# Kernel optimization log

Measured on AMD Instinct MI355X. Metric: run time of the kernel, lower is better.

Reference implementation:

```python
import jax, jax.numpy as jnp
import numpy as np

B, CIN, COUT, K, E, H, W = 32, 128, 256, 3, 8, 64, 64


def setup_inputs() -> dict:
    key = jax.random.key(0)
    k1, k2, k3, k4 = jax.random.split(key, 4)
    x = jax.random.normal(k1, (B, CIN, H, W), dtype=jnp.float32)
    expert_weight = jax.random.normal(k2, (E, COUT, CIN, K, K), dtype=jnp.float32)
    # nn.Linear(in_channels, num_experts): weight [E, CIN], bias [E]
    bound = 1.0 / np.sqrt(CIN)
    routing_w = jax.random.uniform(k3, (E, CIN), minval=-bound, maxval=bound, dtype=jnp.float32)
    routing_b = jax.random.uniform(k4, (E,), minval=-bound, maxval=bound, dtype=jnp.float32)
    return {"x": x, "expert_weight": expert_weight, "routing_w": routing_w, "routing_b": routing_b}


def reference(x, expert_weight, routing_w, routing_b):
    # routing: global-avg-pool -> linear -> softmax over experts
    pooled = x.mean(axis=(2, 3))                             # [B, CIN]
    logits = pooled @ routing_w.T + routing_b                # [B, E]
    rweights = jax.nn.softmax(logits, axis=-1)               # [B, E]
    # per-sample combined conv weights: [B, COUT, CIN, K, K]
    cw = jnp.einsum('be,eoikl->boikl', rweights, expert_weight)

    def conv_one(xi, wi):
        # xi: [CIN, H, W], wi: [COUT, CIN, K, K]; VALID conv, stride 1
        return jax.lax.conv_general_dilated(
            xi[None], wi, window_strides=(1, 1), padding='VALID',
            dimension_numbers=('NCHW', 'OIHW', 'NCHW'))[0]

    return jax.vmap(conv_one)(x, cw)                         # [B, COUT, H-K+1, W-K+1]
```

## Files before the change

### kernel.cpp

```cpp
#include <hip/hip_runtime.h>
#include <hip/hip_bf16.h>


#define CC_B    32
#define CC_CIN  128
#define CC_COUT 256
#define CC_NP   3844
#define CC_NT   18

typedef __attribute__((ext_vector_type(8))) short bf16x8;
typedef __attribute__((ext_vector_type(16))) float f32x16;

__global__ void cc_nhwc(const float* __restrict__ x, __hip_bfloat16* __restrict__ xn,
                        float* __restrict__ psum) {
    const int b = blockIdx.x >> 6, y = blockIdx.x & 63;
    __shared__ float lds[64 * 129];
    __shared__ float sred[256];
    const int t = threadIdx.x;
    const float* src = x + (size_t)b * CC_CIN * 4096 + y * 64;
#pragma unroll
    for (int i = 0; i < 32; ++i) {
        const int idx = i * 256 + t;
        const int cin = idx >> 6, xx = idx & 63;
        lds[xx * 129 + cin] = src[(size_t)cin * 4096 + xx];
    }
    __syncthreads();
    __hip_bfloat16* dst = xn + ((size_t)b * 4096 + y * 64) * CC_CIN;
#pragma unroll
    for (int j = 0; j < 4; ++j) {
        const int cidx = j * 256 + t;
        const int xx = cidx >> 4, c8 = (cidx & 15) * 8;
        union { __hip_bfloat16 h[8]; uint4 v; } u;
#pragma unroll
        for (int jj = 0; jj < 8; ++jj) u.h[jj] = __float2bfloat16(lds[xx * 129 + c8 + jj]);
        *reinterpret_cast<uint4*>(dst + (size_t)xx * CC_CIN + c8) = u.v;
    }
    const int cin = t & 127, xh = (t >> 7) * 32;
    float s = 0.f;
#pragma unroll
    for (int xx = 0; xx < 32; ++xx) s += lds[(xh + xx) * 129 + cin];
    sred[t] = s;
    __syncthreads();
    if (t < 128) psum[((size_t)b * 64 + y) * CC_CIN + t] = sred[t] + sred[t + 128];
}

__global__ void cc_route(const float* __restrict__ psum,
                         const float* __restrict__ rw_w,
                         const float* __restrict__ rw_b,
                         float* __restrict__ rweights) {
    const int b = blockIdx.x, c = threadIdx.x;
    __shared__ float pl[128];
    __shared__ float lg[8];
    const float* p = psum + (size_t)b * 64 * CC_CIN + c;
    float s = 0.f;
#pragma unroll 8
    for (int y = 0; y < 64; ++y) s += p[(size_t)y * CC_CIN];
    pl[c] = s * (1.f / 4096.f);
    __syncthreads();
    if (c < 8) {
        const float* w = rw_w + c * CC_CIN;
        float a = rw_b[c];
#pragma unroll 8
        for (int i = 0; i < CC_CIN; ++i) a += pl[i] * w[i];
        lg[c] = a;
    }
    __syncthreads();
    if (c == 0) {
        float m = lg[0];
#pragma unroll
        for (int e = 1; e < 8; ++e) m = fmaxf(m, lg[e]);
        float ex[8], sm = 0.f;
#pragma unroll
        for (int e = 0; e < 8; ++e) { ex[e] = __expf(lg[e] - m); sm += ex[e]; }
#pragma unroll
        for (int e = 0; e < 8; ++e) rweights[b * 8 + e] = ex[e] / sm;
    }
}

__global__ void cc_combine(const float* __restrict__ ew,
                           const float* __restrict__ rw,
                           __hip_bfloat16* __restrict__ cw) {
    const int t9 = blockIdx.x >> 8;
    const int cout = blockIdx.x & 255;
    const int cin = threadIdx.x;
    __shared__ float rws[256];
    rws[cin] = rw[cin];
    rws[cin + 128] = rw[cin + 128];
    __syncthreads();
    float wv[8];
    const size_t base = ((size_t)cout * CC_CIN + cin) * 9 + t9;
#pragma unroll
    for (int e = 0; e < 8; ++e) wv[e] = ew[base + (size_t)e * (CC_COUT * CC_CIN * 9)];
#pragma unroll 4
    for (int b = 0; b < CC_B; ++b) {
        float acc = 0.f;
#pragma unroll
        for (int e = 0; e < 8; ++e) acc += rws[b * 8 + e] * wv[e];
        cw[(((size_t)b * 9 + t9) * CC_COUT + cout) * CC_CIN + cin] = __float2bfloat16(acc);
    }
}

__device__ __forceinline__ void gload_lds16(const void* g, void* l) {
    __builtin_amdgcn_global_load_lds(
        (const __attribute__((address_space(1))) unsigned int*)g,
        (__attribute__((address_space(3))) unsigned int*)l, 16, 0, 0);
}

__global__ __launch_bounds__(256) void cc_conv(
    const __hip_bfloat16* __restrict__ xn,
    const __hip_bfloat16* __restrict__ cw,
    float* __restrict__ out)
{
    __shared__ __align__(16) char smem[65536];
    const int l   = blockIdx.x;
    const int xcd = l & 7, li = l >> 3;
    const int b   = 4 * xcd + li / 62;
    const int r2  = li % 62;
    const int nt  = r2 >> 1, mt = r2 & 1;
    const int m0  = mt * 128;
    const int n0  = nt * 124;
    const int y0  = 2 * nt;

    const int tid = threadIdx.x;
    const int wid = tid >> 6, lane = tid & 63;
    const int waveM = wid >> 1, waveN = wid & 1;

    f32x16 acc[2][2];
#pragma unroll
    for (int i = 0; i < 2; ++i)
#pragma unroll
        for (int j = 0; j < 2; ++j)
#pragma unroll
            for (int v = 0; v < 16; ++v) acc[i][j][v] = 0.f;

    const __hip_bfloat16* cwb = cw + (size_t)b * 9 * CC_COUT * CC_CIN;
    const __hip_bfloat16* xnb = xn + (size_t)b * 4096 * CC_CIN;

    const int aRow = (wid >> 1) * 64 + lane;
    int laOff[4];
#pragma unroll
    for (int i = 0; i < 4; ++i)
        laOff[i] = (m0 + aRow) * CC_CIN + (i * 2 + (wid & 1)) * 8;
    auto stageA = [&](int t) {
        const int h = t / 9, t9 = t - 9 * h;
        const int aoff = t9 * (CC_COUT * CC_CIN) + h * 64;
        char* Ab = smem + (t & 1) * 16384 + (wid >> 1) * 1024;
#pragma unroll
        for (int i = 0; i < 4; ++i)
            gload_lds16(cwb + aoff + laOff[i], Ab + (i * 2 + (wid & 1)) * 2048);
    };

    char* Bres = smem + 32768;
    const int lbOff = ((y0 + wid) * 64 + lane) * CC_CIN;
    auto stageB = [&](int h) {
        char* Bb = Bres + wid * 1024;
#pragma unroll
        for (int i = 0; i < 8; ++i)
            gload_lds16(xnb + lbOff + i * 8 + h * 64, Bb + i * 4096);
    };

    const int l31 = lane & 31, q2 = lane >> 5;

    int pixB[2];
#pragma unroll
    for (int nf = 0; nf < 2; ++nf) {
        int c = nf * 32 + l31;
        if (c > 61) c = 61;
        pixB[nf] = waveN * 64 + c;
    }

    stageB(0);
    stageA(0);
    stageA(1);

#pragma unroll
    for (int t = 0; t < CC_NT; ++t) {
        const int h = t / 9, t9 = t - 9 * h;
        const int kyx = (t9 / 3) * 64 + (t9 - 3 * (t9 / 3));
        const char* Ab = smem + (t & 1) * 16384;

        if (t < CC_NT - 1) asm volatile("s_waitcnt vmcnt(4)" ::: "memory");
        else               asm volatile("s_waitcnt vmcnt(0)" ::: "memory");
        asm volatile("s_barrier" ::: "memory");

        bf16x8 af[2][4], bf[2][4];
#pragma unroll
        for (int ks = 0; ks < 4; ++ks) {
            const int c = ks * 2 + q2;
#pragma unroll
            for (int mf = 0; mf < 2; ++mf) {
                const int r = waveM * 64 + mf * 32 + l31;
                af[mf][ks] = *(const bf16x8*)(Ab + c * 2048 + r * 16);
            }
#pragma unroll
            for (int nf = 0; nf < 2; ++nf) {
                const int row = pixB[nf] + kyx;
                bf[nf][ks] = *(const bf16x8*)(Bres + c * 4096 + row * 16);
            }
        }
        __builtin_amdgcn_s_setprio(1);
#pragma unroll
        for (int ks = 0; ks < 4; ++ks)
#pragma unroll
            for (int mf = 0; mf < 2; ++mf)
#pragma unroll
                for (int nf = 0; nf < 2; ++nf)
                    acc[mf][nf] = __builtin_amdgcn_mfma_f32_32x32x16_bf16(
                        af[mf][ks], bf[nf][ks], acc[mf][nf], 0, 0, 0);
        __builtin_amdgcn_s_setprio(0);

        asm volatile("s_waitcnt lgkmcnt(0)" ::: "memory");
        asm volatile("s_barrier" ::: "memory");
        if (t == 8) stageB(1);
        if (t + 2 < CC_NT) stageA(t + 2);
    }

#pragma unroll
    for (int mf = 0; mf < 2; ++mf) {
#pragma unroll
        for (int nf = 0; nf < 2; ++nf) {
            const int c2 = nf * 32 + l31;
            if (c2 < 62) {
                const int p = n0 + waveN * 62 + c2;
#pragma unroll
                for (int g = 0; g < 4; ++g) {
                    const int crow = m0 + waveM * 64 + mf * 32 + g * 8 + q2 * 4;
                    const size_t ob = ((size_t)b * CC_COUT + crow) * CC_NP + p;
#pragma unroll
                    for (int j = 0; j < 4; ++j)
                        out[ob + (size_t)j * CC_NP] = acc[mf][nf][g * 4 + j];
                }
            }
        }
    }
}

extern "C" void kernel_launch(void* const* d_in, const int* in_sizes, int n_in,
                              void* d_out, int out_size, void* d_ws, size_t ws_size,
                              hipStream_t stream) {
    const float* x   = (const float*)d_in[0];
    const float* ew  = (const float*)d_in[1];
    const float* rww = (const float*)d_in[2];
    const float* rwb = (const float*)d_in[3];
    float* out = (float*)d_out;
    char* ws = (char*)d_ws;

    __hip_bfloat16* xnhwc = (__hip_bfloat16*)ws;
    __hip_bfloat16* cwcmb = (__hip_bfloat16*)(ws + 33554432);
    float* psum   = (float*)(ws + 52428800);
    float* rwts   = (float*)(ws + 53493760);

    cc_nhwc<<<dim3(CC_B * 64), dim3(256), 0, stream>>>(x, xnhwc, psum);
    cc_route<<<dim3(CC_B), dim3(128), 0, stream>>>(psum, rww, rwb, rwts);
    cc_combine<<<dim3(9 * CC_COUT), dim3(128), 0, stream>>>(ew, rwts, cwcmb);
    cc_conv<<<dim3(1984), dim3(256), 0, stream>>>(xnhwc, cwcmb, out);
}
```

Measured before the change: 138.9 us.

## Store activations and combined weights in k8-chunked layouts for contiguous LDS loads

Changes the intermediate bf16 activation tensor from NHWC to a [b][cin/8][pixel][8] layout and the combined weight tensor to [b][tap][cin/8][cout][8]. The producer kernels write in these layouts, and the conv kernel's global-to-LDS loads now read contiguous 16-byte chunks across lanes instead of lanes strided by 256 bytes. This is meant to improve coalescing of the direct-to-LDS loads. The combine kernel's stores become more scattered, with 2-byte writes strided per lane, which may cost more in that stage.

```diff
diff --git a/kernel.cpp b/kernel.cpp
--- a/kernel.cpp
+++ b/kernel.cpp
@@ -11,7 +11,7 @@
 typedef __attribute__((ext_vector_type(8))) short bf16x8;
 typedef __attribute__((ext_vector_type(16))) float f32x16;
 
-__global__ void cc_nhwc(const float* __restrict__ x, __hip_bfloat16* __restrict__ xn,
+__global__ void cc_nhwc(const float* __restrict__ x, __hip_bfloat16* __restrict__ xnt,
                         float* __restrict__ psum) {
     const int b = blockIdx.x >> 6, y = blockIdx.x & 63;
     __shared__ float lds[64 * 129];
@@ -25,15 +25,14 @@
         lds[xx * 129 + cin] = src[(size_t)cin * 4096 + xx];
     }
     __syncthreads();
-    __hip_bfloat16* dst = xn + ((size_t)b * 4096 + y * 64) * CC_CIN;
 #pragma unroll
     for (int j = 0; j < 4; ++j) {
         const int cidx = j * 256 + t;
-        const int xx = cidx >> 4, c8 = (cidx & 15) * 8;
+        const int k8 = cidx >> 6, xx = cidx & 63;
         union { __hip_bfloat16 h[8]; uint4 v; } u;
 #pragma unroll
-        for (int jj = 0; jj < 8; ++jj) u.h[jj] = __float2bfloat16(lds[xx * 129 + c8 + jj]);
-        *reinterpret_cast<uint4*>(dst + (size_t)xx * CC_CIN + c8) = u.v;
+        for (int jj = 0; jj < 8; ++jj) u.h[jj] = __float2bfloat16(lds[xx * 129 + k8 * 8 + jj]);
+        *reinterpret_cast<uint4*>(xnt + (((size_t)b * 16 + k8) * 4096 + y * 64 + xx) * 8) = u.v;
     }
     const int cin = t & 127, xh = (t >> 7) * 32;
     float s = 0.f;
@@ -79,7 +78,7 @@
 
 __global__ void cc_combine(const float* __restrict__ ew,
                            const float* __restrict__ rw,
-                           __hip_bfloat16* __restrict__ cw) {
+                           __hip_bfloat16* __restrict__ cwk) {
     const int t9 = blockIdx.x >> 8;
     const int cout = blockIdx.x & 255;
     const int cin = threadIdx.x;
@@ -91,12 +90,14 @@
     const size_t base = ((size_t)cout * CC_CIN + cin) * 9 + t9;
 #pragma unroll
     for (int e = 0; e < 8; ++e) wv[e] = ew[base + (size_t)e * (CC_COUT * CC_CIN * 9)];
+    const int k8 = cin >> 3, jj = cin & 7;
 #pragma unroll 4
     for (int b = 0; b < CC_B; ++b) {
         float acc = 0.f;
 #pragma unroll
         for (int e = 0; e < 8; ++e) acc += rws[b * 8 + e] * wv[e];
-        cw[(((size_t)b * 9 + t9) * CC_COUT + cout) * CC_CIN + cin] = __float2bfloat16(acc);
+        cwk[(size_t)b * 294912 + ((t9 * 16 + k8) * 256 + cout) * 8 + jj]
+            = __float2bfloat16(acc);
     }
 }
 
@@ -107,8 +108,8 @@
 }
 
 __global__ __launch_bounds__(256) void cc_conv(
-    const __hip_bfloat16* __restrict__ xn,
-    const __hip_bfloat16* __restrict__ cw,
+    const __hip_bfloat16* __restrict__ xnt,
+    const __hip_bfloat16* __restrict__ cwk,
     float* __restrict__ out)
 {
     __shared__ __align__(16) char smem[65536];
@@ -133,30 +134,28 @@
 #pragma unroll
             for (int v = 0; v < 16; ++v) acc[i][j][v] = 0.f;
 
-    const __hip_bfloat16* cwb = cw + (size_t)b * 9 * CC_COUT * CC_CIN;
-    const __hip_bfloat16* xnb = xn + (size_t)b * 4096 * CC_CIN;
-
-    const int aRow = (wid >> 1) * 64 + lane;
-    int laOff[4];
-#pragma unroll
-    for (int i = 0; i < 4; ++i)
-        laOff[i] = (m0 + aRow) * CC_CIN + (i * 2 + (wid & 1)) * 8;
+    const __hip_bfloat16* cwb = cwk + (size_t)b * 294912;
+    const __hip_bfloat16* xnb = xnt + (size_t)b * 524288;
+
+    const int aHalf = wid >> 1, aPar = wid & 1;
     auto stageA = [&](int t) {
         const int h = t / 9, t9 = t - 9 * h;
-        const int aoff = t9 * (CC_COUT * CC_CIN) + h * 64;
-        char* Ab = smem + (t & 1) * 16384 + (wid >> 1) * 1024;
-#pragma unroll
-        for (int i = 0; i < 4; ++i)
-            gload_lds16(cwb + aoff + laOff[i], Ab + (i * 2 + (wid & 1)) * 2048);
+        char* Ab = smem + (t & 1) * 16384 + aHalf * 1024;
+#pragma unroll
+        for (int i = 0; i < 4; ++i) {
+            const int p = i * 2 + aPar;
+            gload_lds16(cwb + (((t9 * 16 + h * 8 + p) * 256 + m0 + aHalf * 64 + lane) * 8),
+                        Ab + p * 2048);
+        }
     };
 
     char* Bres = smem + 32768;
-    const int lbOff = ((y0 + wid) * 64 + lane) * CC_CIN;
+    const int bPix = (y0 + wid) * 64 + lane;
     auto stageB = [&](int h) {
         char* Bb = Bres + wid * 1024;
 #pragma unroll
         for (int i = 0; i < 8; ++i)
-            gload_lds16(xnb + lbOff + i * 8 + h * 64, Bb + i * 4096);
+            gload_lds16(xnb + (((size_t)(h * 8 + i) * 4096 + bPix) * 8), Bb + i * 4096);
     };
 
     const int l31 = lane & 31, q2 = lane >> 5;
@@ -245,13 +244,13 @@
     float* out = (float*)d_out;
     char* ws = (char*)d_ws;
 
-    __hip_bfloat16* xnhwc = (__hip_bfloat16*)ws;
-    __hip_bfloat16* cwcmb = (__hip_bfloat16*)(ws + 33554432);
+    __hip_bfloat16* xnt   = (__hip_bfloat16*)ws;
+    __hip_bfloat16* cwkb  = (__hip_bfloat16*)(ws + 33554432);
     float* psum   = (float*)(ws + 52428800);
     float* rwts   = (float*)(ws + 53493760);
 
-    cc_nhwc<<<dim3(CC_B * 64), dim3(256), 0, stream>>>(x, xnhwc, psum);
+    cc_nhwc<<<dim3(CC_B * 64), dim3(256), 0, stream>>>(x, xnt, psum);
     cc_route<<<dim3(CC_B), dim3(128), 0, stream>>>(psum, rww, rwb, rwts);
-    cc_combine<<<dim3(9 * CC_COUT), dim3(128), 0, stream>>>(ew, rwts, cwcmb);
-    cc_conv<<<dim3(1984), dim3(256), 0, stream>>>(xnhwc, cwcmb, out);
-}
+    cc_combine<<<dim3(9 * CC_COUT), dim3(128), 0, stream>>>(ew, rwts, cwkb);
+    cc_conv<<<dim3(1984), dim3(256), 0, stream>>>(xnt, cwkb, out);
+}
```

After: 127.3 us. 8.4% less time.
